# Performance work log

Measured on AMD Instinct MI355X. Metric: run time of the kernel, lower is better.

The kernel has to match this reference:

```python
import jax, jax.numpy as jnp
import numpy as np

CX = 256  # args.Cx in the original repo (hidden channel dim)

def setup_inputs() -> dict:
    key = jax.random.key(0)
    kK, kV, kQ = jax.random.split(key, 3)
    N, Cx, Tx, Ty = 16, CX, 2048, 2048
    K = jax.random.normal(kK, (N, Cx, Tx), dtype=jnp.float32)
    V = jax.random.normal(kV, (N, Cx, Tx), dtype=jnp.float32)
    Q = jax.random.normal(kQ, (N, Cx, Ty), dtype=jnp.float32)
    return {"K": K, "V": V, "Q": Q}

def reference(K, V, Q):
    # scores: (N, Tx, Ty) = K^T Q / sqrt(Cx)
    scale = 1.0 / np.sqrt(CX).astype(np.float32)
    scores = jnp.einsum('nct,ncy->nty', K, Q) * scale
    A = jax.nn.softmax(scores, axis=1)          # softmax over Tx (dim=1)
    R = jnp.einsum('nct,nty->ncy', V, A)         # (N, Cx, Ty)
    return (R, A)
```

## Files before the change

### kernel.cpp

```cpp
#include <hip/hip_runtime.h>

#define NB 16
#define CX 256
#define TX 2048
#define TY 2048
#define SCALE 0.0625f

typedef __attribute__((ext_vector_type(8))) short short8;
typedef __attribute__((ext_vector_type(4))) short short4v;
typedef __attribute__((ext_vector_type(4))) float floatx4;

__device__ float L_dev[NB * TY];

static __device__ __forceinline__ short f2bf(float x) {
#if defined(__gfx950__)
    __bf16 b = (__bf16)x;
    return __builtin_bit_cast(short, b);
#else
    union { float f; unsigned u; } v; v.f = x;
    unsigned r = v.u + 0x7fff + ((v.u >> 16) & 1);
    return (short)(r >> 16);
#endif
}

__global__ __launch_bounds__(256) void k_prep(const float* __restrict__ K,
                                              const float* __restrict__ Q,
                                              short* __restrict__ KT,
                                              short* __restrict__ QT) {
    __shared__ float Tsh[32][36];
    const int tid = threadIdx.x;
    const int t0  = blockIdx.x * 32;
    const int c0  = blockIdx.y * 32;
    const int isQ = blockIdx.z & 1;
    const int n   = blockIdx.z >> 1;
    const float* src = (isQ ? Q : K) + (size_t)n * CX * TX;
    short*       dst = (isQ ? QT : KT) + (size_t)n * TX * CX;
    const float scale = isQ ? 1.0f : SCALE;

    const int r  = tid >> 3;
    const int q4 = (tid & 7) * 4;
    *(floatx4*)&Tsh[r][q4] =
        *(const floatx4*)(src + (size_t)(c0 + r) * TX + t0 + q4);
    __syncthreads();
    short4v o = { f2bf(Tsh[q4 + 0][r] * scale),
                  f2bf(Tsh[q4 + 1][r] * scale),
                  f2bf(Tsh[q4 + 2][r] * scale),
                  f2bf(Tsh[q4 + 3][r] * scale) };
    *(short4v*)(dst + (size_t)(t0 + r) * CX + c0 + q4) = o;
}

__global__ __launch_bounds__(256) void k_zero() {
    L_dev[blockIdx.x * 256 + threadIdx.x] = 0.f;
}

__global__ __launch_bounds__(256) void k_scores2(const short* __restrict__ KT,
                                                 const short* __restrict__ QT,
                                                 float* __restrict__ E) {
    __shared__ short Ksh[128][40];
    __shared__ short Qsh[128][40];
    __shared__ float Lsh[128];
    const int tid = threadIdx.x;
    const int n  = blockIdx.z;
    const int t0 = blockIdx.y * 128;
    const int y0 = blockIdx.x * 128;

    const short* Ka = KT + ((size_t)n * TX + t0) * CX;
    const short* Qa = QT + ((size_t)n * TY + y0) * CX;

    if (tid < 128) Lsh[tid] = 0.f;

    const int sr = tid >> 1;
    const int sc = (tid & 1) * 16;
    const short* Kp = Ka + (size_t)sr * CX + sc;
    const short* Qp = Qa + (size_t)sr * CX + sc;

    const int lane = tid & 63;
    const int w    = tid >> 6;
    const int wy   = (w >> 1) * 64;
    const int wt   = (w & 1) * 64;
    const int fr   = lane & 15;
    const int fq   = lane >> 4;

    floatx4 acc[4][4];
#pragma unroll
    for (int i = 0; i < 4; ++i)
#pragma unroll
        for (int j = 0; j < 4; ++j) acc[i][j] = (floatx4)0.f;

    short8 ra0 = *(const short8*)(Kp + 0);
    short8 ra1 = *(const short8*)(Kp + 8);
    short8 rb0 = *(const short8*)(Qp + 0);
    short8 rb1 = *(const short8*)(Qp + 8);

    for (int k0 = 0; k0 < CX; k0 += 32) {
        *(short8*)&Ksh[sr][sc]     = ra0;
        *(short8*)&Ksh[sr][sc + 8] = ra1;
        *(short8*)&Qsh[sr][sc]     = rb0;
        *(short8*)&Qsh[sr][sc + 8] = rb1;
        __syncthreads();
        if (k0 + 32 < CX) {
            ra0 = *(const short8*)(Kp + k0 + 32);
            ra1 = *(const short8*)(Kp + k0 + 40);
            rb0 = *(const short8*)(Qp + k0 + 32);
            rb1 = *(const short8*)(Qp + k0 + 40);
        }
        short8 af[4], bv[4];
#pragma unroll
        for (int mt = 0; mt < 4; ++mt)
            af[mt] = *(short8*)&Qsh[wy + mt * 16 + fr][fq * 8];
#pragma unroll
        for (int nt = 0; nt < 4; ++nt)
            bv[nt] = *(short8*)&Ksh[wt + nt * 16 + fr][fq * 8];
#pragma unroll
        for (int mt = 0; mt < 4; ++mt)
#pragma unroll
            for (int nt = 0; nt < 4; ++nt)
                acc[mt][nt] = __builtin_amdgcn_mfma_f32_16x16x32_bf16(
                    af[mt], bv[nt], acc[mt][nt], 0, 0, 0);
        __syncthreads();
    }

    float* Ep = E + (size_t)n * TX * TY;
#pragma unroll
    for (int nt = 0; nt < 4; ++nt) {
        const size_t trow = (size_t)(t0 + wt + nt * 16 + fr) * TY;
#pragma unroll
        for (int mt = 0; mt < 4; ++mt) {
            floatx4 e;
#pragma unroll
            for (int c = 0; c < 4; ++c) e[c] = __expf(acc[mt][nt][c]);
            acc[mt][nt] = e;
            *(floatx4*)&Ep[trow + y0 + wy + mt * 16 + fq * 4] = e;
        }
    }

#pragma unroll
    for (int mt = 0; mt < 4; ++mt) {
#pragma unroll
        for (int reg = 0; reg < 4; ++reg) {
            float v = 0.f;
#pragma unroll
            for (int nt = 0; nt < 4; ++nt) v += acc[mt][nt][reg];
            v += __shfl_xor(v, 1);
            v += __shfl_xor(v, 2);
            v += __shfl_xor(v, 4);
            v += __shfl_xor(v, 8);
            if (fr == 0) atomicAdd(&Lsh[wy + mt * 16 + fq * 4 + reg], v);
        }
    }
    __syncthreads();
    if (tid < 128) atomicAdd(&L_dev[(size_t)n * TY + y0 + tid], Lsh[tid]);
}

__global__ __launch_bounds__(256) void k_pv3(const float* __restrict__ V,
                                             float* __restrict__ EA,
                                             float* __restrict__ R) {
    __shared__ short Vsh[256][40];
    __shared__ short Psh[64][40];
    const int tid = threadIdx.x;
    const int n  = blockIdx.y;
    const int y0 = blockIdx.x * 64;

    const float* Vp = V + (size_t)n * CX * TX;
    float* Ap = EA + (size_t)n * TX * TY + y0;
    float* Rp = R + (size_t)n * CX * TY;

    const int tt = tid & 7;
    const int tc = tid >> 3;
    const int sy = tid & 63;
    const int kh = tid >> 6;

    const float inv = 1.0f / L_dev[(size_t)n * TY + y0 + sy];

    const int lane = tid & 63;
    const int w    = tid >> 6;
    const int wc   = w * 64;
    const int fr   = lane & 15;
    const int fq   = lane >> 4;

    floatx4 acc[4][4];
#pragma unroll
    for (int i = 0; i < 4; ++i)
#pragma unroll
        for (int j = 0; j < 4; ++j) acc[i][j] = (floatx4)0.f;

    floatx4 rv[8];
    float   ra[8];
#pragma unroll
    for (int cc = 0; cc < 8; ++cc)
        rv[cc] = *(const floatx4*)(Vp + (size_t)(cc * 32 + tc) * TX + tt * 4);
#pragma unroll
    for (int j = 0; j < 8; ++j)
        ra[j] = Ap[(size_t)(kh * 8 + j) * TY + sy];

    for (int k0 = 0; k0 < TX; k0 += 32) {
        float a[8];
#pragma unroll
        for (int j = 0; j < 8; ++j) a[j] = ra[j] * inv;
#pragma unroll
        for (int j = 0; j < 8; ++j)
            Ap[(size_t)(k0 + kh * 8 + j) * TY + sy] = a[j];
        short8 ps = { f2bf(a[0]), f2bf(a[1]), f2bf(a[2]), f2bf(a[3]),
                      f2bf(a[4]), f2bf(a[5]), f2bf(a[6]), f2bf(a[7]) };
        *(short8*)&Psh[sy][kh * 8] = ps;
#pragma unroll
        for (int cc = 0; cc < 8; ++cc) {
            short4v sv = {f2bf(rv[cc][0]), f2bf(rv[cc][1]),
                          f2bf(rv[cc][2]), f2bf(rv[cc][3])};
            *(short4v*)&Vsh[cc * 32 + tc][tt * 4] = sv;
        }
        __syncthreads();
        if (k0 + 32 < TX) {
            const int k1 = k0 + 32;
#pragma unroll
            for (int cc = 0; cc < 8; ++cc)
                rv[cc] = *(const floatx4*)(Vp + (size_t)(cc * 32 + tc) * TX +
                                           k1 + tt * 4);
#pragma unroll
            for (int j = 0; j < 8; ++j)
                ra[j] = Ap[(size_t)(k1 + kh * 8 + j) * TY + sy];
        }
        short8 af[4], bv[4];
#pragma unroll
        for (int mt = 0; mt < 4; ++mt)
            af[mt] = *(short8*)&Psh[mt * 16 + fr][fq * 8];
#pragma unroll
        for (int nt = 0; nt < 4; ++nt)
            bv[nt] = *(short8*)&Vsh[wc + nt * 16 + fr][fq * 8];
#pragma unroll
        for (int mt = 0; mt < 4; ++mt)
#pragma unroll
            for (int nt = 0; nt < 4; ++nt)
                acc[mt][nt] = __builtin_amdgcn_mfma_f32_16x16x32_bf16(
                    af[mt], bv[nt], acc[mt][nt], 0, 0, 0);
        __syncthreads();
    }

#pragma unroll
    for (int nt = 0; nt < 4; ++nt) {
        const size_t crow = (size_t)(wc + nt * 16 + fr) * TY;
#pragma unroll
        for (int mt = 0; mt < 4; ++mt)
            *(floatx4*)&Rp[crow + y0 + mt * 16 + fq * 4] = acc[mt][nt];
    }
}

extern "C" void kernel_launch(void* const* d_in, const int* in_sizes, int n_in,
                              void* d_out, int out_size, void* d_ws, size_t ws_size,
                              hipStream_t stream) {
    (void)in_sizes; (void)n_in; (void)out_size; (void)d_ws; (void)ws_size;
    const float* K = (const float*)d_in[0];
    const float* V = (const float*)d_in[1];
    const float* Q = (const float*)d_in[2];
    float* R = (float*)d_out;
    float* A = (float*)d_out + (size_t)NB * CX * TY;
    short* KT = (short*)d_out;
    short* QT = KT + (size_t)NB * TX * CX;

    dim3 blk(256);
    k_prep   <<<dim3(TX / 32, CX / 32, NB * 2), blk, 0, stream>>>(K, Q, KT, QT);
    k_zero   <<<dim3(NB * TY / 256), blk, 0, stream>>>();
    k_scores2<<<dim3(TY / 128, TX / 128, NB), blk, 0, stream>>>(KT, QT, A);
    k_pv3    <<<dim3(TY / 64, NB), blk, 0, stream>>>(V, A, R);
}
```

Baseline: 590.7 us.

## Double-buffer LDS in scores and PV kernels, pre-convert V to bf16

Both GEMM kernels now use two LDS buffers, so the next tile is written while the current one is consumed, which removes one barrier per k-step. A new kernel converts V to bf16 once into a device global buffer. The PV kernel then reads half the bytes for V and skips repeated per-block conversion. This costs an extra 16 MB bf16 buffer plus another launch and pass over V, and doubles LDS use per block, which may lower occupancy.

```diff
diff --git a/kernel.cpp b/kernel.cpp
--- a/kernel.cpp
+++ b/kernel.cpp
@@ -11,6 +11,7 @@
 typedef __attribute__((ext_vector_type(4))) float floatx4;
 
 __device__ float L_dev[NB * TY];
+__device__ short Vb_dev[(size_t)NB * CX * TX];
 
 static __device__ __forceinline__ short f2bf(float x) {
 #if defined(__gfx950__)
@@ -49,6 +50,15 @@
     *(short4v*)(dst + (size_t)(t0 + r) * CX + c0 + q4) = o;
 }
 
+__global__ __launch_bounds__(256) void k_prepv(const float* __restrict__ V) {
+    const size_t i = ((size_t)blockIdx.x * 256 + threadIdx.x) * 8;
+    floatx4 v0 = *(const floatx4*)(V + i);
+    floatx4 v1 = *(const floatx4*)(V + i + 4);
+    short8 o = { f2bf(v0[0]), f2bf(v0[1]), f2bf(v0[2]), f2bf(v0[3]),
+                 f2bf(v1[0]), f2bf(v1[1]), f2bf(v1[2]), f2bf(v1[3]) };
+    *(short8*)(Vb_dev + i) = o;
+}
+
 __global__ __launch_bounds__(256) void k_zero() {
     L_dev[blockIdx.x * 256 + threadIdx.x] = 0.f;
 }
@@ -56,8 +66,8 @@
 __global__ __launch_bounds__(256) void k_scores2(const short* __restrict__ KT,
                                                  const short* __restrict__ QT,
                                                  float* __restrict__ E) {
-    __shared__ short Ksh[128][40];
-    __shared__ short Qsh[128][40];
+    __shared__ short Ksh[2][128][40];
+    __shared__ short Qsh[2][128][40];
     __shared__ float Lsh[128];
     const int tid = threadIdx.x;
     const int n  = blockIdx.z;
@@ -91,26 +101,38 @@
     short8 ra1 = *(const short8*)(Kp + 8);
     short8 rb0 = *(const short8*)(Qp + 0);
     short8 rb1 = *(const short8*)(Qp + 8);
-
-    for (int k0 = 0; k0 < CX; k0 += 32) {
-        *(short8*)&Ksh[sr][sc]     = ra0;
-        *(short8*)&Ksh[sr][sc + 8] = ra1;
-        *(short8*)&Qsh[sr][sc]     = rb0;
-        *(short8*)&Qsh[sr][sc + 8] = rb1;
-        __syncthreads();
-        if (k0 + 32 < CX) {
-            ra0 = *(const short8*)(Kp + k0 + 32);
-            ra1 = *(const short8*)(Kp + k0 + 40);
-            rb0 = *(const short8*)(Qp + k0 + 32);
-            rb1 = *(const short8*)(Qp + k0 + 40);
+    *(short8*)&Ksh[0][sr][sc]     = ra0;
+    *(short8*)&Ksh[0][sr][sc + 8] = ra1;
+    *(short8*)&Qsh[0][sr][sc]     = rb0;
+    *(short8*)&Qsh[0][sr][sc + 8] = rb1;
+    ra0 = *(const short8*)(Kp + 32);
+    ra1 = *(const short8*)(Kp + 40);
+    rb0 = *(const short8*)(Qp + 32);
+    rb1 = *(const short8*)(Qp + 40);
+    __syncthreads();
+
+    for (int i = 0; i < 8; ++i) {
+        const int cur = i & 1, nxt = cur ^ 1;
+        if (i < 7) {
+            *(short8*)&Ksh[nxt][sr][sc]     = ra0;
+            *(short8*)&Ksh[nxt][sr][sc + 8] = ra1;
+            *(short8*)&Qsh[nxt][sr][sc]     = rb0;
+            *(short8*)&Qsh[nxt][sr][sc + 8] = rb1;
+            if (i < 6) {
+                const int k2 = (i + 2) * 32;
+                ra0 = *(const short8*)(Kp + k2);
+                ra1 = *(const short8*)(Kp + k2 + 8);
+                rb0 = *(const short8*)(Qp + k2);
+                rb1 = *(const short8*)(Qp + k2 + 8);
+            }
         }
         short8 af[4], bv[4];
 #pragma unroll
         for (int mt = 0; mt < 4; ++mt)
-            af[mt] = *(short8*)&Qsh[wy + mt * 16 + fr][fq * 8];
+            af[mt] = *(short8*)&Qsh[cur][wy + mt * 16 + fr][fq * 8];
 #pragma unroll
         for (int nt = 0; nt < 4; ++nt)
-            bv[nt] = *(short8*)&Ksh[wt + nt * 16 + fr][fq * 8];
+            bv[nt] = *(short8*)&Ksh[cur][wt + nt * 16 + fr][fq * 8];
 #pragma unroll
         for (int mt = 0; mt < 4; ++mt)
 #pragma unroll
@@ -152,23 +174,22 @@
     if (tid < 128) atomicAdd(&L_dev[(size_t)n * TY + y0 + tid], Lsh[tid]);
 }
 
-__global__ __launch_bounds__(256) void k_pv3(const float* __restrict__ V,
-                                             float* __restrict__ EA,
+__global__ __launch_bounds__(256) void k_pv4(float* __restrict__ EA,
                                              float* __restrict__ R) {
-    __shared__ short Vsh[256][40];
-    __shared__ short Psh[64][40];
+    __shared__ short Vsh[2][256][40];
+    __shared__ short Psh[2][64][40];
     const int tid = threadIdx.x;
     const int n  = blockIdx.y;
     const int y0 = blockIdx.x * 64;
 
-    const float* Vp = V + (size_t)n * CX * TX;
+    const short* Vbn = Vb_dev + (size_t)n * CX * TX;
     float* Ap = EA + (size_t)n * TX * TY + y0;
     float* Rp = R + (size_t)n * CX * TY;
 
-    const int tt = tid & 7;
-    const int tc = tid >> 3;
     const int sy = tid & 63;
-    const int kh = tid >> 6;
+    const int kq = tid >> 6;
+    const int tv = tid & 3;
+    const int rv = tid >> 2;
 
     const float inv = 1.0f / L_dev[(size_t)n * TY + y0 + sy];
 
@@ -184,49 +205,71 @@
 #pragma unroll
         for (int j = 0; j < 4; ++j) acc[i][j] = (floatx4)0.f;
 
-    floatx4 rv[8];
-    float   ra[8];
-#pragma unroll
-    for (int cc = 0; cc < 8; ++cc)
-        rv[cc] = *(const floatx4*)(Vp + (size_t)(cc * 32 + tc) * TX + tt * 4);
+    float  rE[8];
+    short8 rV[4];
+
 #pragma unroll
     for (int j = 0; j < 8; ++j)
-        ra[j] = Ap[(size_t)(kh * 8 + j) * TY + sy];
-
-    for (int k0 = 0; k0 < TX; k0 += 32) {
+        rE[j] = Ap[(size_t)(kq * 8 + j) * TY + sy];
+#pragma unroll
+    for (int jj = 0; jj < 4; ++jj)
+        rV[jj] = *(const short8*)(Vbn + (size_t)(rv + jj * 64) * TX + tv * 8);
+    {
         float a[8];
 #pragma unroll
-        for (int j = 0; j < 8; ++j) a[j] = ra[j] * inv;
+        for (int j = 0; j < 8; ++j) a[j] = rE[j] * inv;
 #pragma unroll
         for (int j = 0; j < 8; ++j)
-            Ap[(size_t)(k0 + kh * 8 + j) * TY + sy] = a[j];
+            Ap[(size_t)(kq * 8 + j) * TY + sy] = a[j];
         short8 ps = { f2bf(a[0]), f2bf(a[1]), f2bf(a[2]), f2bf(a[3]),
                       f2bf(a[4]), f2bf(a[5]), f2bf(a[6]), f2bf(a[7]) };
-        *(short8*)&Psh[sy][kh * 8] = ps;
-#pragma unroll
-        for (int cc = 0; cc < 8; ++cc) {
-            short4v sv = {f2bf(rv[cc][0]), f2bf(rv[cc][1]),
-                          f2bf(rv[cc][2]), f2bf(rv[cc][3])};
-            *(short4v*)&Vsh[cc * 32 + tc][tt * 4] = sv;
-        }
-        __syncthreads();
-        if (k0 + 32 < TX) {
-            const int k1 = k0 + 32;
-#pragma unroll
-            for (int cc = 0; cc < 8; ++cc)
-                rv[cc] = *(const floatx4*)(Vp + (size_t)(cc * 32 + tc) * TX +
-                                           k1 + tt * 4);
+        *(short8*)&Psh[0][sy][kq * 8] = ps;
+#pragma unroll
+        for (int jj = 0; jj < 4; ++jj)
+            *(short8*)&Vsh[0][rv + jj * 64][tv * 8] = rV[jj];
+    }
+#pragma unroll
+    for (int j = 0; j < 8; ++j)
+        rE[j] = Ap[(size_t)(32 + kq * 8 + j) * TY + sy];
+#pragma unroll
+    for (int jj = 0; jj < 4; ++jj)
+        rV[jj] = *(const short8*)(Vbn + (size_t)(rv + jj * 64) * TX + 32 + tv * 8);
+    __syncthreads();
+
+    for (int i = 0; i < TX / 32; ++i) {
+        const int cur = i & 1, nxt = cur ^ 1;
+        if (i < 63) {
+            const int t1 = (i + 1) * 32;
+            float a[8];
+#pragma unroll
+            for (int j = 0; j < 8; ++j) a[j] = rE[j] * inv;
 #pragma unroll
             for (int j = 0; j < 8; ++j)
-                ra[j] = Ap[(size_t)(k1 + kh * 8 + j) * TY + sy];
+                Ap[(size_t)(t1 + kq * 8 + j) * TY + sy] = a[j];
+            short8 ps = { f2bf(a[0]), f2bf(a[1]), f2bf(a[2]), f2bf(a[3]),
+                          f2bf(a[4]), f2bf(a[5]), f2bf(a[6]), f2bf(a[7]) };
+            *(short8*)&Psh[nxt][sy][kq * 8] = ps;
+#pragma unroll
+            for (int jj = 0; jj < 4; ++jj)
+                *(short8*)&Vsh[nxt][rv + jj * 64][tv * 8] = rV[jj];
+            if (i < 62) {
+                const int t2 = (i + 2) * 32;
+#pragma unroll
+                for (int j = 0; j < 8; ++j)
+                    rE[j] = Ap[(size_t)(t2 + kq * 8 + j) * TY + sy];
+#pragma unroll
+                for (int jj = 0; jj < 4; ++jj)
+                    rV[jj] = *(const short8*)(Vbn +
+                               (size_t)(rv + jj * 64) * TX + t2 + tv * 8);
+            }
         }
         short8 af[4], bv[4];
 #pragma unroll
         for (int mt = 0; mt < 4; ++mt)
-            af[mt] = *(short8*)&Psh[mt * 16 + fr][fq * 8];
+            af[mt] = *(short8*)&Psh[cur][mt * 16 + fr][fq * 8];
 #pragma unroll
         for (int nt = 0; nt < 4; ++nt)
-            bv[nt] = *(short8*)&Vsh[wc + nt * 16 + fr][fq * 8];
+            bv[nt] = *(short8*)&Vsh[cur][wc + nt * 16 + fr][fq * 8];
 #pragma unroll
         for (int mt = 0; mt < 4; ++mt)
 #pragma unroll
@@ -259,7 +302,8 @@
 
     dim3 blk(256);
     k_prep   <<<dim3(TX / 32, CX / 32, NB * 2), blk, 0, stream>>>(K, Q, KT, QT);
+    k_prepv  <<<dim3((NB * CX * TX) / (256 * 8)), blk, 0, stream>>>(V);
     k_zero   <<<dim3(NB * TY / 256), blk, 0, stream>>>();
     k_scores2<<<dim3(TY / 128, TX / 128, NB), blk, 0, stream>>>(KT, QT, A);
-    k_pv3    <<<dim3(TY / 64, NB), blk, 0, stream>>>(V, A, R);
-}
+    k_pv4    <<<dim3(TY / 64, NB), blk, 0, stream>>>(A, R);
+}
```

After: 592.3 us. About the same (+0.3%).

## Pre-convert V to bf16 and halve the PV tile width for more blocks

Applied to the files above, without the earlier changes.

Adds a separate kernel that converts V to bf16 once into a global buffer, so the PV kernel loads bf16 V directly instead of converting fp32 in every block. The PV kernel tile shrinks from 64 to 32 output columns, doubling the grid to 1024 blocks, which raises parallelism but means each block re-reads the full bf16 V slice twice as often. The normalized A store is also moved after the barrier. This trades an extra 32MB pass plus more total V traffic for less conversion work and better occupancy.

```diff
diff --git a/kernel.cpp b/kernel.cpp
--- a/kernel.cpp
+++ b/kernel.cpp
@@ -11,6 +11,7 @@
 typedef __attribute__((ext_vector_type(4))) float floatx4;
 
 __device__ float L_dev[NB * TY];
+__device__ __align__(16) short Vb_dev[(size_t)NB * CX * TX];
 
 static __device__ __forceinline__ short f2bf(float x) {
 #if defined(__gfx950__)
@@ -49,6 +50,15 @@
     *(short4v*)(dst + (size_t)(t0 + r) * CX + c0 + q4) = o;
 }
 
+__global__ __launch_bounds__(256) void k_prepv(const float* __restrict__ V) {
+    const size_t i = ((size_t)blockIdx.x * 256 + threadIdx.x) * 8;
+    floatx4 v0 = *(const floatx4*)(V + i);
+    floatx4 v1 = *(const floatx4*)(V + i + 4);
+    short8 o = { f2bf(v0[0]), f2bf(v0[1]), f2bf(v0[2]), f2bf(v0[3]),
+                 f2bf(v1[0]), f2bf(v1[1]), f2bf(v1[2]), f2bf(v1[3]) };
+    *(short8*)(Vb_dev + i) = o;
+}
+
 __global__ __launch_bounds__(256) void k_zero() {
     L_dev[blockIdx.x * 256 + threadIdx.x] = 0.f;
 }
@@ -152,23 +162,22 @@
     if (tid < 128) atomicAdd(&L_dev[(size_t)n * TY + y0 + tid], Lsh[tid]);
 }
 
-__global__ __launch_bounds__(256) void k_pv3(const float* __restrict__ V,
-                                             float* __restrict__ EA,
+__global__ __launch_bounds__(256) void k_pv5(float* __restrict__ EA,
                                              float* __restrict__ R) {
     __shared__ short Vsh[256][40];
-    __shared__ short Psh[64][40];
+    __shared__ short Psh[32][40];
     const int tid = threadIdx.x;
     const int n  = blockIdx.y;
-    const int y0 = blockIdx.x * 64;
-
-    const float* Vp = V + (size_t)n * CX * TX;
+    const int y0 = blockIdx.x * 32;
+
+    const short* Vbn = Vb_dev + (size_t)n * CX * TX;
     float* Ap = EA + (size_t)n * TX * TY + y0;
     float* Rp = R + (size_t)n * CX * TY;
 
-    const int tt = tid & 7;
-    const int tc = tid >> 3;
-    const int sy = tid & 63;
-    const int kh = tid >> 6;
+    const int sy = tid & 31;
+    const int kq = tid >> 5;
+    const int tv = tid & 3;
+    const int rv = tid >> 2;
 
     const float inv = 1.0f / L_dev[(size_t)n * TY + y0 + sy];
 
@@ -178,57 +187,55 @@
     const int fr   = lane & 15;
     const int fq   = lane >> 4;
 
-    floatx4 acc[4][4];
-#pragma unroll
-    for (int i = 0; i < 4; ++i)
+    floatx4 acc[2][4];
+#pragma unroll
+    for (int i = 0; i < 2; ++i)
 #pragma unroll
         for (int j = 0; j < 4; ++j) acc[i][j] = (floatx4)0.f;
 
-    floatx4 rv[8];
-    float   ra[8];
-#pragma unroll
-    for (int cc = 0; cc < 8; ++cc)
-        rv[cc] = *(const floatx4*)(Vp + (size_t)(cc * 32 + tc) * TX + tt * 4);
-#pragma unroll
-    for (int j = 0; j < 8; ++j)
-        ra[j] = Ap[(size_t)(kh * 8 + j) * TY + sy];
-
-    for (int k0 = 0; k0 < TX; k0 += 32) {
-        float a[8];
-#pragma unroll
-        for (int j = 0; j < 8; ++j) a[j] = ra[j] * inv;
-#pragma unroll
-        for (int j = 0; j < 8; ++j)
-            Ap[(size_t)(k0 + kh * 8 + j) * TY + sy] = a[j];
-        short8 ps = { f2bf(a[0]), f2bf(a[1]), f2bf(a[2]), f2bf(a[3]),
-                      f2bf(a[4]), f2bf(a[5]), f2bf(a[6]), f2bf(a[7]) };
-        *(short8*)&Psh[sy][kh * 8] = ps;
-#pragma unroll
-        for (int cc = 0; cc < 8; ++cc) {
-            short4v sv = {f2bf(rv[cc][0]), f2bf(rv[cc][1]),
-                          f2bf(rv[cc][2]), f2bf(rv[cc][3])};
-            *(short4v*)&Vsh[cc * 32 + tc][tt * 4] = sv;
-        }
-        __syncthreads();
-        if (k0 + 32 < TX) {
+    float  rE[4];
+    short8 rV[4];
+
+#pragma unroll
+    for (int j = 0; j < 4; ++j)
+        rE[j] = Ap[(size_t)(kq * 4 + j) * TY + sy];
+#pragma unroll
+    for (int jj = 0; jj < 4; ++jj)
+        rV[jj] = *(const short8*)(Vbn + (size_t)(rv + jj * 64) * TX + tv * 8);
+
+    for (int i = 0; i < TX / 32; ++i) {
+        const int k0 = i * 32;
+        float a[4];
+#pragma unroll
+        for (int j = 0; j < 4; ++j) a[j] = rE[j] * inv;
+        short4v ps = { f2bf(a[0]), f2bf(a[1]), f2bf(a[2]), f2bf(a[3]) };
+        *(short4v*)&Psh[sy][kq * 4] = ps;
+#pragma unroll
+        for (int jj = 0; jj < 4; ++jj)
+            *(short8*)&Vsh[rv + jj * 64][tv * 8] = rV[jj];
+        __syncthreads();
+#pragma unroll
+        for (int j = 0; j < 4; ++j)
+            Ap[(size_t)(k0 + kq * 4 + j) * TY + sy] = a[j];
+        if (i < TX / 32 - 1) {
             const int k1 = k0 + 32;
 #pragma unroll
-            for (int cc = 0; cc < 8; ++cc)
-                rv[cc] = *(const floatx4*)(Vp + (size_t)(cc * 32 + tc) * TX +
-                                           k1 + tt * 4);
-#pragma unroll
-            for (int j = 0; j < 8; ++j)
-                ra[j] = Ap[(size_t)(k1 + kh * 8 + j) * TY + sy];
-        }
-        short8 af[4], bv[4];
-#pragma unroll
-        for (int mt = 0; mt < 4; ++mt)
+            for (int j = 0; j < 4; ++j)
+                rE[j] = Ap[(size_t)(k1 + kq * 4 + j) * TY + sy];
+#pragma unroll
+            for (int jj = 0; jj < 4; ++jj)
+                rV[jj] = *(const short8*)(Vbn + (size_t)(rv + jj * 64) * TX +
+                                          k1 + tv * 8);
+        }
+        short8 af[2], bv[4];
+#pragma unroll
+        for (int mt = 0; mt < 2; ++mt)
             af[mt] = *(short8*)&Psh[mt * 16 + fr][fq * 8];
 #pragma unroll
         for (int nt = 0; nt < 4; ++nt)
             bv[nt] = *(short8*)&Vsh[wc + nt * 16 + fr][fq * 8];
 #pragma unroll
-        for (int mt = 0; mt < 4; ++mt)
+        for (int mt = 0; mt < 2; ++mt)
 #pragma unroll
             for (int nt = 0; nt < 4; ++nt)
                 acc[mt][nt] = __builtin_amdgcn_mfma_f32_16x16x32_bf16(
@@ -240,7 +247,7 @@
     for (int nt = 0; nt < 4; ++nt) {
         const size_t crow = (size_t)(wc + nt * 16 + fr) * TY;
 #pragma unroll
-        for (int mt = 0; mt < 4; ++mt)
+        for (int mt = 0; mt < 2; ++mt)
             *(floatx4*)&Rp[crow + y0 + mt * 16 + fq * 4] = acc[mt][nt];
     }
 }
@@ -259,7 +266,8 @@
 
     dim3 blk(256);
     k_prep   <<<dim3(TX / 32, CX / 32, NB * 2), blk, 0, stream>>>(K, Q, KT, QT);
+    k_prepv  <<<dim3((NB * CX * TX) / (256 * 8)), blk, 0, stream>>>(V);
     k_zero   <<<dim3(NB * TY / 256), blk, 0, stream>>>();
     k_scores2<<<dim3(TY / 128, TX / 128, NB), blk, 0, stream>>>(KT, QT, A);
-    k_pv3    <<<dim3(TY / 64, NB), blk, 0, stream>>>(V, A, R);
-}
+    k_pv5    <<<dim3(TY / 32, NB), blk, 0, stream>>>(A, R);
+}
```

Result: slower. 673.7 us (+14.1%).
